# Kernel optimization log

Hardware: AMD Instinct MI355X
Metric: run time of the kernel (lower is better)

## Reference

```python
import jax, jax.numpy as jnp
import numpy as np

N_NODES = 100000
N_EDGES = 3200000
IN_CH = 128
HID = 64
N_CLASSES = 10


def setup_inputs() -> dict:
    key = jax.random.key(0)
    ks = jax.random.split(key, 12)
    def lin(kw, kb, fan_in, fan_out):
        bound = 1.0 / np.sqrt(fan_in)
        W = jax.random.uniform(kw, (fan_in, fan_out), jnp.float32, -bound, bound)
        b = jax.random.uniform(kb, (fan_out,), jnp.float32, -bound, bound)
        return W, b
    x = jax.random.normal(ks[0], (N_NODES, IN_CH), jnp.float32)
    edge_index = jax.random.randint(ks[1], (2, N_EDGES), 0, N_NODES, jnp.int32)
    W1a, b1a = lin(ks[2], ks[3], IN_CH, HID)
    W2a, b2a = lin(ks[4], ks[5], HID, HID)
    W1b, b1b = lin(ks[6], ks[7], HID, HID)
    W2b, b2b = lin(ks[8], ks[9], HID, HID)
    Wl, bl = lin(ks[10], ks[11], HID, N_CLASSES)
    return {"x": x, "edge_index": edge_index,
            "W1a": W1a, "b1a": b1a, "W2a": W2a, "b2a": b2a,
            "W1b": W1b, "b1b": b1b, "W2b": W2b, "b2b": b2b,
            "Wl": Wl, "bl": bl}


def gin_conv(x, src, dst, W1, b1, W2, b2):
    # sum-aggregate neighbor messages: agg[i] = sum_{(src->i)} x[src]
    agg = jax.ops.segment_sum(x[src], dst, num_segments=N_NODES)
    h = agg + x  # (1 + eps) * x with eps = 0 (GINConv default)
    h = jnp.maximum(h @ W1 + b1, 0.0)  # Linear -> ReLU
    return h @ W2 + b2                 # Linear


def reference(x, edge_index, W1a, b1a, W2a, b2a, W1b, b1b, W2b, b2b, Wl, bl):
    src, dst = edge_index[0], edge_index[1]
    h = gin_conv(x, src, dst, W1a, b1a, W2a, b2a)
    h = jnp.maximum(h, 0.0)
    h = gin_conv(h, src, dst, W1b, b1b, W2b, b2b)
    h = jnp.maximum(h, 0.0)
    logits = h @ Wl + bl
    return jax.nn.log_softmax(logits, axis=1)
```

## Files before the change

kernel.cpp:

```cpp
#include <hip/hip_runtime.h>
#include <hip/hip_bf16.h>

#define N_NODES 100000
#define N_EDGES 3200000
#define IN_CH 128
#define HID 64
#define N_CLASSES 10

#define NB 391
#define NPB 256
#define BCAP 10240
#define CHUNK 8192

typedef unsigned short u16;
typedef unsigned int u32;

static __device__ __forceinline__ float u2f(u32 u) {
    union { u32 i; float f; } v; v.i = u; return v.f;
}
static __device__ __forceinline__ u16 f2bf(float f) {
    __hip_bfloat16 b = __float2bfloat16(f);
    return *(u16*)&b;
}


__global__ void __launch_bounds__(1024) passA_k(
        const int* __restrict__ src, const int* __restrict__ dst,
        int* __restrict__ bcnt, u32* __restrict__ stage) {
    __shared__ int lh[NB];
    __shared__ int lb[NB];
    for (int i = threadIdx.x; i < NB; i += 1024) lh[i] = 0;
    __syncthreads();
    int e0 = blockIdx.x * CHUNK;
#pragma unroll
    for (int k = 0; k < CHUNK / 1024; ++k) {
        int e = e0 + k * 1024 + threadIdx.x;
        if (e < N_EDGES) atomicAdd(&lh[dst[e] >> 8], 1);
    }
    __syncthreads();
    for (int i = threadIdx.x; i < NB; i += 1024) {
        lb[i] = atomicAdd(&bcnt[i], lh[i]);
        lh[i] = 0;
    }
    __syncthreads();
#pragma unroll
    for (int k = 0; k < CHUNK / 1024; ++k) {
        int e = e0 + k * 1024 + threadIdx.x;
        if (e < N_EDGES) {
            int d = dst[e];
            int b = d >> 8;
            int p = lb[b] + atomicAdd(&lh[b], 1);
            if (p < BCAP) stage[(size_t)b * BCAP + p] = ((u32)src[e] << 8) | (u32)(d & 255);
        }
    }
}


__global__ void bscan_k(const int* __restrict__ bcnt, int* __restrict__ bbase,
                        int* __restrict__ off) {
    __shared__ int s[512];
    int tid = threadIdx.x;
    int v = (tid < NB) ? min(bcnt[tid], BCAP) : 0;
    s[tid] = v;
    __syncthreads();
    for (int o = 1; o < 512; o <<= 1) {
        int t = (tid >= o) ? s[tid - o] : 0;
        __syncthreads();
        s[tid] += t;
        __syncthreads();
    }
    if (tid < NB) bbase[tid] = s[tid] - v;
    if (tid == NB - 1) off[N_NODES] = s[tid];
}


__global__ void __launch_bounds__(1024) passB_k(
        const int* __restrict__ bcnt, const int* __restrict__ bbase,
        const u32* __restrict__ stage, int* __restrict__ off,
        int* __restrict__ csr) {
    __shared__ int ldeg[NPB];
    __shared__ int loff[NPB + 1];
    __shared__ int lcur[NPB];
    __shared__ int img[BCAP];
    int b = blockIdx.x;
    int nb = min(bcnt[b], BCAP);
    int base = bbase[b];
    const u32* st = stage + (size_t)b * BCAP;
    int tid = threadIdx.x;
    if (tid < NPB) ldeg[tid] = 0;
    __syncthreads();
    for (int i = tid; i < nb; i += 1024) atomicAdd(&ldeg[st[i] & 255u], 1);
    __syncthreads();
    if (tid < NPB) lcur[tid] = ldeg[tid];
    __syncthreads();
    for (int o = 1; o < NPB; o <<= 1) {
        int t = (tid < NPB && tid >= o) ? lcur[tid - o] : 0;
        __syncthreads();
        if (tid < NPB) lcur[tid] += t;
        __syncthreads();
    }
    if (tid < NPB) loff[tid + 1] = lcur[tid];
    if (tid == 0) loff[0] = 0;
    __syncthreads();
    if (tid < NPB) {
        int gnode = (b << 8) + tid;
        if (gnode < N_NODES) off[gnode] = base + loff[tid];
        lcur[tid] = loff[tid];
    }
    __syncthreads();
    for (int i = tid; i < nb; i += 1024) {
        u32 pr = st[i];
        int p = atomicAdd(&lcur[pr & 255u], 1);
        img[p] = (int)(pr >> 8);
    }
    __syncthreads();
    for (int i = tid; i < nb; i += 1024) csr[base + i] = img[i];
}

static __device__ __forceinline__ void fill_swz(float* sW4, const float* __restrict__ W,
                                                int nelem, int tid, int nthr) {
    for (int i = tid; i < nelem; i += nthr) {
        int c = i >> 6, out = i & 63;
        sW4[((c >> 2) << 8) + (out << 2) + (c & 3)] = W[i];
    }
}


__global__ void __launch_bounds__(512) lin1_k(
        const float* __restrict__ x, const float* __restrict__ W1,
        u16* __restrict__ yb) {
    __shared__ __align__(16) float sW4[IN_CH * 64];
    __shared__ __align__(16) float srow[8][IN_CH];
    fill_swz(sW4, W1, IN_CH * 64, threadIdx.x, 512);
    __syncthreads();
    int wid = threadIdx.x >> 6, lane = threadIdx.x & 63;
    int gw = blockIdx.x * 8 + wid;
    const int NW = 1024 * 8;
    for (int n = gw; n < N_NODES; n += NW) {
        srow[wid][lane]      = x[(size_t)n * IN_CH + lane];
        srow[wid][64 + lane] = x[(size_t)n * IN_CH + 64 + lane];
        __builtin_amdgcn_wave_barrier();
        float acc = 0.f;
#pragma unroll
        for (int c4 = 0; c4 < IN_CH / 4; ++c4) {
            float4 w = *(const float4*)&sW4[(c4 << 8) + (lane << 2)];
            float4 r = *(const float4*)&srow[wid][c4 << 2];
            acc = fmaf(r.x, w.x, acc); acc = fmaf(r.y, w.y, acc);
            acc = fmaf(r.z, w.z, acc); acc = fmaf(r.w, w.w, acc);
        }
        __builtin_amdgcn_wave_barrier();
        yb[(size_t)n * 64 + lane] = f2bf(acc);
    }
}

#define AGG_BODY(TAB)                                                                   \
    const char* tb = (const char*)(TAB);                                                \
    int g = lane >> 3, c = lane & 7;                                                    \
    int coff = c << 4;                                     \
    float a0, a1, a2, a3, a4, a5, a6, a7;                                               \
    {   uint4 dS = *(const uint4*)(tb + (size_t)n * 128 + coff);                        \
        u32 sm = (g == 0) ? 0xffffffffu : 0u;                                           \
        dS.x &= sm; dS.y &= sm; dS.z &= sm; dS.w &= sm;                                 \
        a0 = u2f(dS.x << 16); a1 = u2f(dS.x & 0xffff0000u);                             \
        a2 = u2f(dS.y << 16); a3 = u2f(dS.y & 0xffff0000u);                             \
        a4 = u2f(dS.z << 16); a5 = u2f(dS.z & 0xffff0000u);                             \
        a6 = u2f(dS.w << 16); a7 = u2f(dS.w & 0xffff0000u); }                           \
    int e = off[n], e1 = off[n + 1];                                                    \
    int nfull = (e1 - e) >> 3;                                                          \
    _Pragma("unroll 4")                                                                 \
    for (int it = 0; it < nfull; ++it) {                                                \
        int s = csr[e + g];                                                             \
        uint4 d = *(const uint4*)(tb + (size_t)s * 128 + coff);                         \
        a0 += u2f(d.x << 16); a1 += u2f(d.x & 0xffff0000u);                             \
        a2 += u2f(d.y << 16); a3 += u2f(d.y & 0xffff0000u);                             \
        a4 += u2f(d.z << 16); a5 += u2f(d.z & 0xffff0000u);                             \
        a6 += u2f(d.w << 16); a7 += u2f(d.w & 0xffff0000u);                             \
        e += 8;                                                                         \
    }                                                                                   \
    int rem = e1 - e;                                                                   \
    if (rem > 0) {                                                                      \
        int s = csr[e + min(g, rem - 1)];                                               \
        u32 m = (g < rem) ? 0xffffffffu : 0u;                                           \
        uint4 d = *(const uint4*)(tb + (size_t)s * 128 + coff);                         \
        d.x &= m; d.y &= m; d.z &= m; d.w &= m;                                         \
        a0 += u2f(d.x << 16); a1 += u2f(d.x & 0xffff0000u);                             \
        a2 += u2f(d.y << 16); a3 += u2f(d.y & 0xffff0000u);                             \
        a4 += u2f(d.z << 16); a5 += u2f(d.z & 0xffff0000u);                             \
        a6 += u2f(d.w << 16); a7 += u2f(d.w & 0xffff0000u);                             \
    }                                                                                   \
                                     \
    a0 += __shfl_xor(a0, 8);  a1 += __shfl_xor(a1, 8);  a2 += __shfl_xor(a2, 8);        \
    a3 += __shfl_xor(a3, 8);  a4 += __shfl_xor(a4, 8);  a5 += __shfl_xor(a5, 8);        \
    a6 += __shfl_xor(a6, 8);  a7 += __shfl_xor(a7, 8);                                  \
    a0 += __shfl_xor(a0, 16); a1 += __shfl_xor(a1, 16); a2 += __shfl_xor(a2, 16);       \
    a3 += __shfl_xor(a3, 16); a4 += __shfl_xor(a4, 16); a5 += __shfl_xor(a5, 16);       \
    a6 += __shfl_xor(a6, 16); a7 += __shfl_xor(a7, 16);                                 \
    a0 += __shfl_xor(a0, 32); a1 += __shfl_xor(a1, 32); a2 += __shfl_xor(a2, 32);       \
    a3 += __shfl_xor(a3, 32); a4 += __shfl_xor(a4, 32); a5 += __shfl_xor(a5, 32);       \
    a6 += __shfl_xor(a6, 32); a7 += __shfl_xor(a7, 32);


__global__ void __launch_bounds__(512) aggFA_k(
        const u16* __restrict__ yb, const int* __restrict__ off,
        const int* __restrict__ csr, const float* __restrict__ b1,
        const float* __restrict__ W2, const float* __restrict__ b2,
        u16* __restrict__ h1b) {
    __shared__ __align__(16) float sW4[64 * 64];
    __shared__ __align__(16) float su[8][64];
    fill_swz(sW4, W2, 64 * 64, threadIdx.x, 512);
    __syncthreads();
    int wid = threadIdx.x >> 6, lane = threadIdx.x & 63;
    float4 b1v0 = ((const float4*)b1)[(lane & 7) * 2];
    float4 b1v1 = ((const float4*)b1)[(lane & 7) * 2 + 1];
    float bb2 = b2[lane];
    int gw = blockIdx.x * 8 + wid;
    const int NW = 1024 * 8;
    for (int n = gw; n < N_NODES; n += NW) {
        AGG_BODY(yb)
        if (lane < 8) {
            float4 u0 = make_float4(fmaxf(a0 + b1v0.x, 0.f), fmaxf(a1 + b1v0.y, 0.f),
                                    fmaxf(a2 + b1v0.z, 0.f), fmaxf(a3 + b1v0.w, 0.f));
            float4 u1 = make_float4(fmaxf(a4 + b1v1.x, 0.f), fmaxf(a5 + b1v1.y, 0.f),
                                    fmaxf(a6 + b1v1.z, 0.f), fmaxf(a7 + b1v1.w, 0.f));
            *(float4*)&su[wid][c << 3] = u0;
            *(float4*)&su[wid][(c << 3) + 4] = u1;
        }
        __builtin_amdgcn_wave_barrier();
        float o = bb2;
#pragma unroll
        for (int c4 = 0; c4 < 16; ++c4) {
            float4 w = *(const float4*)&sW4[(c4 << 8) + (lane << 2)];
            float4 v = *(const float4*)&su[wid][c4 << 2];
            o = fmaf(w.x, v.x, o); o = fmaf(w.y, v.y, o);
            o = fmaf(w.z, v.z, o); o = fmaf(w.w, v.w, o);
        }
        __builtin_amdgcn_wave_barrier();
        h1b[(size_t)n * 64 + lane] = f2bf(fmaxf(o, 0.f));
    }
}


__global__ void __launch_bounds__(512) aggFB_k(
        const u16* __restrict__ h1b, const int* __restrict__ off,
        const int* __restrict__ csr, const float* __restrict__ W1,
        const float* __restrict__ b1, const float* __restrict__ W2,
        const float* __restrict__ b2, u16* __restrict__ h2b) {
    __shared__ __align__(16) float sW14[64 * 64];
    __shared__ __align__(16) float sW24[64 * 64];
    __shared__ __align__(16) float su1[8][64];
    __shared__ __align__(16) float su2[8][64];
    fill_swz(sW14, W1, 64 * 64, threadIdx.x, 512);
    fill_swz(sW24, W2, 64 * 64, threadIdx.x, 512);
    __syncthreads();
    int wid = threadIdx.x >> 6, lane = threadIdx.x & 63;
    float bb1 = b1[lane], bb2 = b2[lane];
    int gw = blockIdx.x * 8 + wid;
    const int NW = 1024 * 8;
    for (int n = gw; n < N_NODES; n += NW) {
        AGG_BODY(h1b)
        if (lane < 8) {
            *(float4*)&su1[wid][c << 3] = make_float4(a0, a1, a2, a3);
            *(float4*)&su1[wid][(c << 3) + 4] = make_float4(a4, a5, a6, a7);
        }
        __builtin_amdgcn_wave_barrier();
        float u = bb1;
#pragma unroll
        for (int c4 = 0; c4 < 16; ++c4) {
            float4 w = *(const float4*)&sW14[(c4 << 8) + (lane << 2)];
            float4 v = *(const float4*)&su1[wid][c4 << 2];
            u = fmaf(w.x, v.x, u); u = fmaf(w.y, v.y, u);
            u = fmaf(w.z, v.z, u); u = fmaf(w.w, v.w, u);
        }
        u = fmaxf(u, 0.f);
        __builtin_amdgcn_wave_barrier();
        su2[wid][lane] = u;
        __builtin_amdgcn_wave_barrier();
        float o = bb2;
#pragma unroll
        for (int c4 = 0; c4 < 16; ++c4) {
            float4 w = *(const float4*)&sW24[(c4 << 8) + (lane << 2)];
            float4 v = *(const float4*)&su2[wid][c4 << 2];
            o = fmaf(w.x, v.x, o); o = fmaf(w.y, v.y, o);
            o = fmaf(w.z, v.z, o); o = fmaf(w.w, v.w, o);
        }
        __builtin_amdgcn_wave_barrier();
        h2b[(size_t)n * 64 + lane] = f2bf(fmaxf(o, 0.f));
    }
}


__global__ void cls_k(const u16* __restrict__ h2b, const float* __restrict__ Wl,
                      const float* __restrict__ bl, float* __restrict__ out) {
    __shared__ float sW[64 * N_CLASSES];
    __shared__ float sb[16];
    for (int i = threadIdx.x; i < 64 * N_CLASSES; i += 256) sW[i] = Wl[i];
    if (threadIdx.x < N_CLASSES) sb[threadIdx.x] = bl[threadIdx.x];
    __syncthreads();
    int n = blockIdx.x * 256 + threadIdx.x;
    if (n >= N_NODES) return;
    float logit[N_CLASSES];
#pragma unroll
    for (int k = 0; k < N_CLASSES; ++k) logit[k] = sb[k];
    const ushort4* row = (const ushort4*)(h2b + (size_t)n * 64);
#pragma unroll
    for (int i = 0; i < 16; ++i) {
        ushort4 q = row[i];
        float v0 = u2f(((u32)q.x) << 16), v1 = u2f(((u32)q.y) << 16);
        float v2 = u2f(((u32)q.z) << 16), v3 = u2f(((u32)q.w) << 16);
#pragma unroll
        for (int k = 0; k < N_CLASSES; ++k) {
            logit[k] = fmaf(v0, sW[(i * 4 + 0) * N_CLASSES + k], logit[k]);
            logit[k] = fmaf(v1, sW[(i * 4 + 1) * N_CLASSES + k], logit[k]);
            logit[k] = fmaf(v2, sW[(i * 4 + 2) * N_CLASSES + k], logit[k]);
            logit[k] = fmaf(v3, sW[(i * 4 + 3) * N_CLASSES + k], logit[k]);
        }
    }
    float m = logit[0];
#pragma unroll
    for (int k = 1; k < N_CLASSES; ++k) m = fmaxf(m, logit[k]);
    float s = 0.f;
#pragma unroll
    for (int k = 0; k < N_CLASSES; ++k) s = s + __expf(logit[k] - m);
    float ls = __logf(s);
#pragma unroll
    for (int k = 0; k < N_CLASSES; ++k) out[(size_t)n * N_CLASSES + k] = logit[k] - m - ls;
}


extern "C" void kernel_launch(void* const* d_in, const int* in_sizes, int n_in,
                              void* d_out, int out_size, void* d_ws, size_t ws_size,
                              hipStream_t stream) {
    const float* x   = (const float*)d_in[0];
    const int*   ei  = (const int*)d_in[1];
    const int*   src = ei;
    const int*   dst = ei + N_EDGES;
    const float* W1a = (const float*)d_in[2];
    const float* b1a = (const float*)d_in[3];
    const float* W2a = (const float*)d_in[4];
    const float* b2a = (const float*)d_in[5];
    const float* W1b = (const float*)d_in[6];
    const float* b1b = (const float*)d_in[7];
    const float* W2b = (const float*)d_in[8];
    const float* b2b = (const float*)d_in[9];
    const float* Wl  = (const float*)d_in[10];
    const float* bl  = (const float*)d_in[11];
    float* out = (float*)d_out;

    char* ws = (char*)d_ws;
    size_t o = 0;
    auto alloc = [&](size_t bytes) -> void* {
        o = (o + 255) & ~(size_t)255;
        void* p = ws + o;
        o += bytes;
        return p;
    };
    int* bcnt  = (int*)alloc((size_t)NB * 4);
    int* bbase = (int*)alloc((size_t)NB * 4);
    int* off   = (int*)alloc((size_t)(N_NODES + 1) * 4);
    u32* stage = (u32*)alloc((size_t)NB * BCAP * 4);
    int* csr   = (int*)alloc((size_t)N_EDGES * 4);
    u16* yb    = (u16*)alloc((size_t)N_NODES * 64 * 2);
    u16* h1b   = (u16*)alloc((size_t)N_NODES * 64 * 2);
    u16* h2b   = (u16*)alloc((size_t)N_NODES * 64 * 2);

    hipMemsetAsync(bcnt, 0, (size_t)NB * 4, stream);

    const int nA = (N_EDGES + CHUNK - 1) / CHUNK;
    passA_k<<<nA, 1024, 0, stream>>>(src, dst, bcnt, stage);
    bscan_k<<<1, 512, 0, stream>>>(bcnt, bbase, off);
    passB_k<<<NB, 1024, 0, stream>>>(bcnt, bbase, stage, off, csr);

    lin1_k <<<1024, 512, 0, stream>>>(x, W1a, yb);
    aggFA_k<<<1024, 512, 0, stream>>>(yb, off, csr, b1a, W2a, b2a, h1b);
    aggFB_k<<<1024, 512, 0, stream>>>(h1b, off, csr, W1b, b1b, W2b, b2b, h2b);
    cls_k  <<<(N_NODES + 255) / 256, 256, 0, stream>>>(h2b, Wl, bl, out);
}
```

Baseline: 374.0 us.

## Split gather from MLP into separate kernels and fuse classifier into second MLP

Moves the neighbour aggregation out of the two MLP kernels into a standalone gather kernel that writes bf16 sums to a new buffer. The MLP kernels then read the pre-aggregated rows. The classifier and log-softmax are fused into the second MLP kernel, which removes the h2 round trip and one launch. The split keeps the gather kernel free of shared-memory weights, which may raise occupancy for the memory-bound gather. In exchange it adds an extra write and read of an intermediate table per layer, plus an extra bf16 rounding of the aggregated sum.

```diff
diff --git a/kernel.cpp b/kernel.cpp
--- a/kernel.cpp
+++ b/kernel.cpp
@@ -21,6 +21,9 @@
 static __device__ __forceinline__ u16 f2bf(float f) {
     __hip_bfloat16 b = __float2bfloat16(f);
     return *(u16*)&b;
+}
+static __device__ __forceinline__ u32 pack2(float lo, float hi) {
+    return (u32)f2bf(lo) | ((u32)f2bf(hi) << 16);
 }
 
 
@@ -153,56 +156,69 @@
     }
 }
 
-#define AGG_BODY(TAB)                                                                   \
-    const char* tb = (const char*)(TAB);                                                \
-    int g = lane >> 3, c = lane & 7;                                                    \
-    int coff = c << 4;                                     \
-    float a0, a1, a2, a3, a4, a5, a6, a7;                                               \
-    {   uint4 dS = *(const uint4*)(tb + (size_t)n * 128 + coff);                        \
-        u32 sm = (g == 0) ? 0xffffffffu : 0u;                                           \
-        dS.x &= sm; dS.y &= sm; dS.z &= sm; dS.w &= sm;                                 \
-        a0 = u2f(dS.x << 16); a1 = u2f(dS.x & 0xffff0000u);                             \
-        a2 = u2f(dS.y << 16); a3 = u2f(dS.y & 0xffff0000u);                             \
-        a4 = u2f(dS.z << 16); a5 = u2f(dS.z & 0xffff0000u);                             \
-        a6 = u2f(dS.w << 16); a7 = u2f(dS.w & 0xffff0000u); }                           \
-    int e = off[n], e1 = off[n + 1];                                                    \
-    int nfull = (e1 - e) >> 3;                                                          \
-    _Pragma("unroll 4")                                                                 \
-    for (int it = 0; it < nfull; ++it) {                                                \
-        int s = csr[e + g];                                                             \
-        uint4 d = *(const uint4*)(tb + (size_t)s * 128 + coff);                         \
-        a0 += u2f(d.x << 16); a1 += u2f(d.x & 0xffff0000u);                             \
-        a2 += u2f(d.y << 16); a3 += u2f(d.y & 0xffff0000u);                             \
-        a4 += u2f(d.z << 16); a5 += u2f(d.z & 0xffff0000u);                             \
-        a6 += u2f(d.w << 16); a7 += u2f(d.w & 0xffff0000u);                             \
-        e += 8;                                                                         \
-    }                                                                                   \
-    int rem = e1 - e;                                                                   \
-    if (rem > 0) {                                                                      \
-        int s = csr[e + min(g, rem - 1)];                                               \
-        u32 m = (g < rem) ? 0xffffffffu : 0u;                                           \
-        uint4 d = *(const uint4*)(tb + (size_t)s * 128 + coff);                         \
-        d.x &= m; d.y &= m; d.z &= m; d.w &= m;                                         \
-        a0 += u2f(d.x << 16); a1 += u2f(d.x & 0xffff0000u);                             \
-        a2 += u2f(d.y << 16); a3 += u2f(d.y & 0xffff0000u);                             \
-        a4 += u2f(d.z << 16); a5 += u2f(d.z & 0xffff0000u);                             \
-        a6 += u2f(d.w << 16); a7 += u2f(d.w & 0xffff0000u);                             \
-    }                                                                                   \
-                                     \
-    a0 += __shfl_xor(a0, 8);  a1 += __shfl_xor(a1, 8);  a2 += __shfl_xor(a2, 8);        \
-    a3 += __shfl_xor(a3, 8);  a4 += __shfl_xor(a4, 8);  a5 += __shfl_xor(a5, 8);        \
-    a6 += __shfl_xor(a6, 8);  a7 += __shfl_xor(a7, 8);                                  \
-    a0 += __shfl_xor(a0, 16); a1 += __shfl_xor(a1, 16); a2 += __shfl_xor(a2, 16);       \
-    a3 += __shfl_xor(a3, 16); a4 += __shfl_xor(a4, 16); a5 += __shfl_xor(a5, 16);       \
-    a6 += __shfl_xor(a6, 16); a7 += __shfl_xor(a7, 16);                                 \
-    a0 += __shfl_xor(a0, 32); a1 += __shfl_xor(a1, 32); a2 += __shfl_xor(a2, 32);       \
-    a3 += __shfl_xor(a3, 32); a4 += __shfl_xor(a4, 32); a5 += __shfl_xor(a5, 32);       \
-    a6 += __shfl_xor(a6, 32); a7 += __shfl_xor(a7, 32);
-
-
-__global__ void __launch_bounds__(512) aggFA_k(
-        const u16* __restrict__ yb, const int* __restrict__ off,
-        const int* __restrict__ csr, const float* __restrict__ b1,
+
+__global__ void __launch_bounds__(512) gather_k(
+        const u16* __restrict__ tab, const int* __restrict__ off,
+        const int* __restrict__ csr, u16* __restrict__ outb) {
+    int wid = threadIdx.x >> 6, lane = threadIdx.x & 63;
+    int g = lane >> 3, c = lane & 7;
+    int coff = c << 4;
+    const char* tb = (const char*)tab;
+    int gw = blockIdx.x * 8 + wid;
+    const int NW = 1024 * 8;
+    for (int n = gw; n < N_NODES; n += NW) {
+        float a0, a1, a2, a3, a4, a5, a6, a7;
+        {
+            uint4 dS = *(const uint4*)(tb + (size_t)n * 128 + coff);
+            u32 sm = (g == 0) ? 0xffffffffu : 0u;
+            dS.x &= sm; dS.y &= sm; dS.z &= sm; dS.w &= sm;
+            a0 = u2f(dS.x << 16); a1 = u2f(dS.x & 0xffff0000u);
+            a2 = u2f(dS.y << 16); a3 = u2f(dS.y & 0xffff0000u);
+            a4 = u2f(dS.z << 16); a5 = u2f(dS.z & 0xffff0000u);
+            a6 = u2f(dS.w << 16); a7 = u2f(dS.w & 0xffff0000u);
+        }
+        int e = off[n], e1 = off[n + 1];
+        int nfull = (e1 - e) >> 3;
+#pragma unroll 4
+        for (int it = 0; it < nfull; ++it) {
+            int s = csr[e + g];
+            uint4 d = *(const uint4*)(tb + (size_t)s * 128 + coff);
+            a0 += u2f(d.x << 16); a1 += u2f(d.x & 0xffff0000u);
+            a2 += u2f(d.y << 16); a3 += u2f(d.y & 0xffff0000u);
+            a4 += u2f(d.z << 16); a5 += u2f(d.z & 0xffff0000u);
+            a6 += u2f(d.w << 16); a7 += u2f(d.w & 0xffff0000u);
+            e += 8;
+        }
+        int rem = e1 - e;
+        if (rem > 0) {
+            int s = csr[e + min(g, rem - 1)];
+            u32 m = (g < rem) ? 0xffffffffu : 0u;
+            uint4 d = *(const uint4*)(tb + (size_t)s * 128 + coff);
+            d.x &= m; d.y &= m; d.z &= m; d.w &= m;
+            a0 += u2f(d.x << 16); a1 += u2f(d.x & 0xffff0000u);
+            a2 += u2f(d.y << 16); a3 += u2f(d.y & 0xffff0000u);
+            a4 += u2f(d.z << 16); a5 += u2f(d.z & 0xffff0000u);
+            a6 += u2f(d.w << 16); a7 += u2f(d.w & 0xffff0000u);
+        }
+        a0 += __shfl_xor(a0, 8);  a1 += __shfl_xor(a1, 8);  a2 += __shfl_xor(a2, 8);
+        a3 += __shfl_xor(a3, 8);  a4 += __shfl_xor(a4, 8);  a5 += __shfl_xor(a5, 8);
+        a6 += __shfl_xor(a6, 8);  a7 += __shfl_xor(a7, 8);
+        a0 += __shfl_xor(a0, 16); a1 += __shfl_xor(a1, 16); a2 += __shfl_xor(a2, 16);
+        a3 += __shfl_xor(a3, 16); a4 += __shfl_xor(a4, 16); a5 += __shfl_xor(a5, 16);
+        a6 += __shfl_xor(a6, 16); a7 += __shfl_xor(a7, 16);
+        a0 += __shfl_xor(a0, 32); a1 += __shfl_xor(a1, 32); a2 += __shfl_xor(a2, 32);
+        a3 += __shfl_xor(a3, 32); a4 += __shfl_xor(a4, 32); a5 += __shfl_xor(a5, 32);
+        a6 += __shfl_xor(a6, 32); a7 += __shfl_xor(a7, 32);
+        if (g == 0) {
+            uint4 pk = make_uint4(pack2(a0, a1), pack2(a2, a3), pack2(a4, a5), pack2(a6, a7));
+            *(uint4*)((char*)outb + (size_t)n * 128 + coff) = pk;
+        }
+    }
+}
+
+
+__global__ void __launch_bounds__(512) mlpA_k(
+        const u16* __restrict__ gab, const float* __restrict__ b1,
         const float* __restrict__ W2, const float* __restrict__ b2,
         u16* __restrict__ h1b) {
     __shared__ __align__(16) float sW4[64 * 64];
@@ -210,18 +226,23 @@
     fill_swz(sW4, W2, 64 * 64, threadIdx.x, 512);
     __syncthreads();
     int wid = threadIdx.x >> 6, lane = threadIdx.x & 63;
-    float4 b1v0 = ((const float4*)b1)[(lane & 7) * 2];
-    float4 b1v1 = ((const float4*)b1)[(lane & 7) * 2 + 1];
+    int g = lane >> 3, c = lane & 7;
+    float4 b1v0 = ((const float4*)b1)[c * 2];
+    float4 b1v1 = ((const float4*)b1)[c * 2 + 1];
     float bb2 = b2[lane];
     int gw = blockIdx.x * 8 + wid;
     const int NW = 1024 * 8;
     for (int n = gw; n < N_NODES; n += NW) {
-        AGG_BODY(yb)
-        if (lane < 8) {
-            float4 u0 = make_float4(fmaxf(a0 + b1v0.x, 0.f), fmaxf(a1 + b1v0.y, 0.f),
-                                    fmaxf(a2 + b1v0.z, 0.f), fmaxf(a3 + b1v0.w, 0.f));
-            float4 u1 = make_float4(fmaxf(a4 + b1v1.x, 0.f), fmaxf(a5 + b1v1.y, 0.f),
-                                    fmaxf(a6 + b1v1.z, 0.f), fmaxf(a7 + b1v1.w, 0.f));
+        if (g == 0) {
+            uint4 d = *(const uint4*)((const char*)gab + (size_t)n * 128 + (c << 4));
+            float4 u0 = make_float4(fmaxf(u2f(d.x << 16) + b1v0.x, 0.f),
+                                    fmaxf(u2f(d.x & 0xffff0000u) + b1v0.y, 0.f),
+                                    fmaxf(u2f(d.y << 16) + b1v0.z, 0.f),
+                                    fmaxf(u2f(d.y & 0xffff0000u) + b1v0.w, 0.f));
+            float4 u1 = make_float4(fmaxf(u2f(d.z << 16) + b1v1.x, 0.f),
+                                    fmaxf(u2f(d.z & 0xffff0000u) + b1v1.y, 0.f),
+                                    fmaxf(u2f(d.w << 16) + b1v1.z, 0.f),
+                                    fmaxf(u2f(d.w & 0xffff0000u) + b1v1.w, 0.f));
             *(float4*)&su[wid][c << 3] = u0;
             *(float4*)&su[wid][(c << 3) + 4] = u1;
         }
@@ -240,27 +261,36 @@
 }
 
 
-__global__ void __launch_bounds__(512) aggFB_k(
-        const u16* __restrict__ h1b, const int* __restrict__ off,
-        const int* __restrict__ csr, const float* __restrict__ W1,
+__global__ void __launch_bounds__(512) mlpBcls_k(
+        const u16* __restrict__ gbb, const float* __restrict__ W1,
         const float* __restrict__ b1, const float* __restrict__ W2,
-        const float* __restrict__ b2, u16* __restrict__ h2b) {
+        const float* __restrict__ b2, const float* __restrict__ Wl,
+        const float* __restrict__ bl, float* __restrict__ out) {
     __shared__ __align__(16) float sW14[64 * 64];
     __shared__ __align__(16) float sW24[64 * 64];
+    __shared__ float sWl[64 * N_CLASSES];
+    __shared__ float sbl[16];
     __shared__ __align__(16) float su1[8][64];
     __shared__ __align__(16) float su2[8][64];
     fill_swz(sW14, W1, 64 * 64, threadIdx.x, 512);
     fill_swz(sW24, W2, 64 * 64, threadIdx.x, 512);
+    for (int i = threadIdx.x; i < 64 * N_CLASSES; i += 512) sWl[i] = Wl[i];
+    if (threadIdx.x < N_CLASSES) sbl[threadIdx.x] = bl[threadIdx.x];
     __syncthreads();
     int wid = threadIdx.x >> 6, lane = threadIdx.x & 63;
+    int g = lane >> 3, c = lane & 7;
     float bb1 = b1[lane], bb2 = b2[lane];
     int gw = blockIdx.x * 8 + wid;
     const int NW = 1024 * 8;
     for (int n = gw; n < N_NODES; n += NW) {
-        AGG_BODY(h1b)
-        if (lane < 8) {
-            *(float4*)&su1[wid][c << 3] = make_float4(a0, a1, a2, a3);
-            *(float4*)&su1[wid][(c << 3) + 4] = make_float4(a4, a5, a6, a7);
+        if (g == 0) {
+            uint4 d = *(const uint4*)((const char*)gbb + (size_t)n * 128 + (c << 4));
+            *(float4*)&su1[wid][c << 3] =
+                make_float4(u2f(d.x << 16), u2f(d.x & 0xffff0000u),
+                            u2f(d.y << 16), u2f(d.y & 0xffff0000u));
+            *(float4*)&su1[wid][(c << 3) + 4] =
+                make_float4(u2f(d.z << 16), u2f(d.z & 0xffff0000u),
+                            u2f(d.w << 16), u2f(d.w & 0xffff0000u));
         }
         __builtin_amdgcn_wave_barrier();
         float u = bb1;
@@ -283,47 +313,31 @@
             o = fmaf(w.x, v.x, o); o = fmaf(w.y, v.y, o);
             o = fmaf(w.z, v.z, o); o = fmaf(w.w, v.w, o);
         }
-        __builtin_amdgcn_wave_barrier();
-        h2b[(size_t)n * 64 + lane] = f2bf(fmaxf(o, 0.f));
-    }
-}
-
-
-__global__ void cls_k(const u16* __restrict__ h2b, const float* __restrict__ Wl,
-                      const float* __restrict__ bl, float* __restrict__ out) {
-    __shared__ float sW[64 * N_CLASSES];
-    __shared__ float sb[16];
-    for (int i = threadIdx.x; i < 64 * N_CLASSES; i += 256) sW[i] = Wl[i];
-    if (threadIdx.x < N_CLASSES) sb[threadIdx.x] = bl[threadIdx.x];
-    __syncthreads();
-    int n = blockIdx.x * 256 + threadIdx.x;
-    if (n >= N_NODES) return;
-    float logit[N_CLASSES];
-#pragma unroll
-    for (int k = 0; k < N_CLASSES; ++k) logit[k] = sb[k];
-    const ushort4* row = (const ushort4*)(h2b + (size_t)n * 64);
-#pragma unroll
-    for (int i = 0; i < 16; ++i) {
-        ushort4 q = row[i];
-        float v0 = u2f(((u32)q.x) << 16), v1 = u2f(((u32)q.y) << 16);
-        float v2 = u2f(((u32)q.z) << 16), v3 = u2f(((u32)q.w) << 16);
-#pragma unroll
-        for (int k = 0; k < N_CLASSES; ++k) {
-            logit[k] = fmaf(v0, sW[(i * 4 + 0) * N_CLASSES + k], logit[k]);
-            logit[k] = fmaf(v1, sW[(i * 4 + 1) * N_CLASSES + k], logit[k]);
-            logit[k] = fmaf(v2, sW[(i * 4 + 2) * N_CLASSES + k], logit[k]);
-            logit[k] = fmaf(v3, sW[(i * 4 + 3) * N_CLASSES + k], logit[k]);
-        }
-    }
-    float m = logit[0];
-#pragma unroll
-    for (int k = 1; k < N_CLASSES; ++k) m = fmaxf(m, logit[k]);
-    float s = 0.f;
-#pragma unroll
-    for (int k = 0; k < N_CLASSES; ++k) s = s + __expf(logit[k] - m);
-    float ls = __logf(s);
-#pragma unroll
-    for (int k = 0; k < N_CLASSES; ++k) out[(size_t)n * N_CLASSES + k] = logit[k] - m - ls;
+        float h2 = fmaxf(o, 0.f);
+        __builtin_amdgcn_wave_barrier();
+        su1[wid][lane] = h2;
+        __builtin_amdgcn_wave_barrier();
+        float logit = -3.0e38f;
+        if (lane < N_CLASSES) {
+            logit = sbl[lane];
+#pragma unroll 8
+            for (int cc = 0; cc < 64; ++cc)
+                logit = fmaf(su1[wid][cc], sWl[cc * N_CLASSES + lane], logit);
+        }
+        float m = logit;
+        m = fmaxf(m, __shfl_xor(m, 1, 16));
+        m = fmaxf(m, __shfl_xor(m, 2, 16));
+        m = fmaxf(m, __shfl_xor(m, 4, 16));
+        m = fmaxf(m, __shfl_xor(m, 8, 16));
+        float ex = (lane < N_CLASSES) ? __expf(logit - m) : 0.f;
+        float s = ex;
+        s += __shfl_xor(s, 1, 16);
+        s += __shfl_xor(s, 2, 16);
+        s += __shfl_xor(s, 4, 16);
+        s += __shfl_xor(s, 8, 16);
+        float ls = __logf(s);
+        if (lane < N_CLASSES) out[(size_t)n * N_CLASSES + lane] = logit - m - ls;
+    }
 }
 
 
@@ -360,8 +374,9 @@
     u32* stage = (u32*)alloc((size_t)NB * BCAP * 4);
     int* csr   = (int*)alloc((size_t)N_EDGES * 4);
     u16* yb    = (u16*)alloc((size_t)N_NODES * 64 * 2);
+    u16* ga    = (u16*)alloc((size_t)N_NODES * 64 * 2);
     u16* h1b   = (u16*)alloc((size_t)N_NODES * 64 * 2);
-    u16* h2b   = (u16*)alloc((size_t)N_NODES * 64 * 2);
+    u16* gb    = (u16*)alloc((size_t)N_NODES * 64 * 2);
 
     hipMemsetAsync(bcnt, 0, (size_t)NB * 4, stream);
 
@@ -370,8 +385,9 @@
     bscan_k<<<1, 512, 0, stream>>>(bcnt, bbase, off);
     passB_k<<<NB, 1024, 0, stream>>>(bcnt, bbase, stage, off, csr);
 
-    lin1_k <<<1024, 512, 0, stream>>>(x, W1a, yb);
-    aggFA_k<<<1024, 512, 0, stream>>>(yb, off, csr, b1a, W2a, b2a, h1b);
-    aggFB_k<<<1024, 512, 0, stream>>>(h1b, off, csr, W1b, b1b, W2b, b2b, h2b);
-    cls_k  <<<(N_NODES + 255) / 256, 256, 0, stream>>>(h2b, Wl, bl, out);
-}
+    lin1_k   <<<1024, 512, 0, stream>>>(x, W1a, yb);
+    gather_k <<<1024, 512, 0, stream>>>(yb, off, csr, ga);
+    mlpA_k   <<<1024, 512, 0, stream>>>(ga, b1a, W2a, b2a, h1b);
+    gather_k <<<1024, 512, 0, stream>>>(h1b, off, csr, gb);
+    mlpBcls_k<<<1024, 512, 0, stream>>>(gb, W1b, b1b, W2b, b2b, Wl, bl, out);
+}
```

New measurement: 452.6 us. 1.21x slower.
